# Kernel optimization log

Hardware: AMD Instinct MI355X
Metric: run time of the kernel (lower is better)

## Reference

```python
import jax, jax.numpy as jnp
import numpy as np

B, T, D, H, C = 256, 256, 512, 1024, 128  # batch, steps, input_size, hidden, num_classes


def setup_inputs() -> dict:
    key = jax.random.key(0)
    ks = jax.random.split(key, 8)
    gru_inputs = jax.random.normal(ks[0], (B, T, D), dtype=jnp.float32)
    true_ids = jax.random.randint(ks[1], (B, T), 0, C)
    true_seq = jax.nn.one_hot(true_ids, C, dtype=jnp.float32)
    s = 1.0 / np.sqrt(H).astype(np.float32)
    W_ih = jax.random.uniform(ks[2], (3 * H, D + C), jnp.float32, -s, s)
    b_ih = jax.random.uniform(ks[3], (3 * H,), jnp.float32, -s, s)
    W_hh = jax.random.uniform(ks[4], (3 * H, H), jnp.float32, -s, s)
    b_hh = jax.random.uniform(ks[5], (3 * H,), jnp.float32, -s, s)
    W_out = jax.random.uniform(ks[6], (C, H), jnp.float32, -s, s)
    b_out = jax.random.uniform(ks[7], (C,), jnp.float32, -s, s)
    return {"gru_inputs": gru_inputs, "true_seq": true_seq, "W_ih": W_ih,
            "b_ih": b_ih, "W_hh": W_hh, "b_hh": b_hh, "W_out": W_out, "b_out": b_out}


def reference(gru_inputs, true_seq, W_ih, b_ih, W_hh, b_hh, W_out, b_out):
    # Teacher-forcing (training) branch of TerminalGRU, dropout=0, bos_idx=None.
    Bb, Tt, _ = gru_inputs.shape
    Cc = true_seq.shape[-1]
    Hh = W_hh.shape[1]
    # prev_y[t] = true_seq[t-1], prev_y[0] = zeros (no BOS)
    prev_y = jnp.concatenate(
        [jnp.zeros((Bb, 1, Cc), gru_inputs.dtype), true_seq[:, :-1]], axis=1)
    inp = jnp.concatenate([gru_inputs, prev_y], axis=-1)  # (B,T,D+C)
    # Precompute input-side gate projections as one big GEMM (faithful math).
    gates_x = jnp.einsum('btd,gd->btg', inp, W_ih) + b_ih  # (B,T,3H)
    xr, xz, xn = jnp.split(gates_x, 3, axis=-1)

    def step(h, xs):
        xr_t, xz_t, xn_t = xs  # each (B,H)
        gh = h @ W_hh.T + b_hh  # (B,3H)
        hr, hz, hn = jnp.split(gh, 3, axis=-1)
        r = jax.nn.sigmoid(xr_t + hr)
        z = jax.nn.sigmoid(xz_t + hz)
        n = jnp.tanh(xn_t + r * hn)
        h_new = (1.0 - z) * n + z * h
        return h_new, h_new

    h0 = jnp.zeros((Bb, Hh), gru_inputs.dtype)
    xs = (xr.transpose(1, 0, 2), xz.transpose(1, 0, 2), xn.transpose(1, 0, 2))
    _, hs = jax.lax.scan(step, h0, xs)  # hs: (T,B,H)
    logits = jnp.einsum('tbh,ch->btc', hs, W_out) + b_out  # (B,T,C)
    return logits
```

## Files before the change

kernel.cpp:

```cpp
#include <hip/hip_runtime.h>


#define DEVI __device__ __forceinline__

typedef __bf16 bf16x8 __attribute__((ext_vector_type(8)));
typedef float f32x4 __attribute__((ext_vector_type(4)));
typedef unsigned long long u64;

static constexpr int Bb = 256, Tt = 256, Dd = 512, Hh = 1024, Cc = 128;
static constexpr int G3 = 3072, DC = 640, TC = 32, NC = Tt / TC;
static constexpr int SLOTS = TC + 1;
static constexpr int LDP = 72;

DEVI unsigned short f2b(float f) {
  union { float f; unsigned u; } v; v.f = f;
  unsigned r = v.u + 0x7FFFu + ((v.u >> 16) & 1u);
  return (unsigned short)(r >> 16);
}
DEVI float b2f(unsigned short h) {
  union { unsigned u; float f; } v; v.u = ((unsigned)h) << 16; return v.f;
}


__global__ __launch_bounds__(256) void k_cvt(const float* __restrict__ x,
                                             unsigned short* __restrict__ o, int n) {
  int i = (blockIdx.x * 256 + threadIdx.x) * 8;
  if (i >= n) return;
  float4 a = *(const float4*)(x + i), b = *(const float4*)(x + i + 4);
  uint4 u;
  u.x = (unsigned)f2b(a.x) | ((unsigned)f2b(a.y) << 16);
  u.y = (unsigned)f2b(a.z) | ((unsigned)f2b(a.w) << 16);
  u.z = (unsigned)f2b(b.x) | ((unsigned)f2b(b.y) << 16);
  u.w = (unsigned)f2b(b.z) | ((unsigned)f2b(b.w) << 16);
  *(uint4*)(o + i) = u;
}

__global__ __launch_bounds__(256) void k_cvt_wa(const float* __restrict__ Wih,
                                                unsigned short* __restrict__ Wa) {
  int u = blockIdx.x * 256 + threadIdx.x;
  int g = u >> 6, d = (u & 63) * 8;
  const float* p = Wih + (size_t)g * DC + d;
  float4 a = *(const float4*)p, b = *(const float4*)(p + 4);
  uint4 o;
  o.x = (unsigned)f2b(a.x) | ((unsigned)f2b(a.y) << 16);
  o.y = (unsigned)f2b(a.z) | ((unsigned)f2b(a.w) << 16);
  o.z = (unsigned)f2b(b.x) | ((unsigned)f2b(b.y) << 16);
  o.w = (unsigned)f2b(b.z) | ((unsigned)f2b(b.w) << 16);
  *(uint4*)(Wa + (size_t)g * Dd + d) = o;
}

__global__ __launch_bounds__(256) void k_cvt_wct(const float* __restrict__ Wih,
                                                 unsigned short* __restrict__ WcT) {
  int g = blockIdx.x * 256 + threadIdx.x;
  int c = blockIdx.y;
  WcT[(size_t)c * G3 + g] = f2b(Wih[(size_t)g * DC + Dd + c]);
}

__global__ __launch_bounds__(256) void k_pid(const float* __restrict__ ts,
                                             int* __restrict__ pid) {
  int bt = blockIdx.x * 256 + threadIdx.x;
  int t = bt & (Tt - 1);
  if (t == 0) { pid[bt] = -1; return; }
  const float* p = ts + (size_t)(bt - 1) * Cc;
  int id = 0;
  for (int c = 0; c < Cc; c += 4) {
    float4 v = *(const float4*)(p + c);
    if (v.x > 0.5f) id = c;
    if (v.y > 0.5f) id = c + 1;
    if (v.z > 0.5f) id = c + 2;
    if (v.w > 0.5f) id = c + 3;
  }
  pid[bt] = id;
}

DEVI void gates_tile(int mi, int ni, const unsigned short* __restrict__ Xb,
                     const unsigned short* __restrict__ Wa,
                     const unsigned short* __restrict__ WcT,
                     const float* __restrict__ bih,
                     const int* __restrict__ pid,
                     unsigned short* __restrict__ gx, int t0c,
                     unsigned short* sA, unsigned short* sB) {
  const int m0 = mi * 128, n0 = ni * 128;
  const int tid = threadIdx.x;
  const int l = tid & 63, w = tid >> 6;
  const int wm = w >> 1, wn = w & 1;
  const int r0l = 64 * wm, c0l = 64 * wn;
  const int lr = l & 15, lk = (l >> 4) * 8;

  int srow[4], sq[4];
  size_t gA[4], gB[4];
#pragma unroll
  for (int c = 0; c < 4; ++c) {
    int ch = tid + c * 256;
    srow[c] = ch >> 3; sq[c] = ch & 7;
    int mrow = m0 + srow[c];
    gA[c] = ((size_t)((mrow >> 5) * Tt + t0c + (mrow & 31))) * Dd + sq[c] * 8;
    gB[c] = (size_t)(n0 + srow[c]) * Dd + sq[c] * 8;
  }

  f32x4 acc[4][4] = {};
  for (int ks = 0; ks < 8; ++ks) {
    int k0 = ks * 64;
    __syncthreads();
#pragma unroll
    for (int c = 0; c < 4; ++c) {
      bf16x8 av = *(const bf16x8*)(Xb + gA[c] + k0);
      bf16x8 bv = *(const bf16x8*)(Wa + gB[c] + k0);
      *(bf16x8*)(sA + srow[c] * LDP + sq[c] * 8) = av;
      *(bf16x8*)(sB + srow[c] * LDP + sq[c] * 8) = bv;
    }
    __syncthreads();
#pragma unroll
    for (int kk = 0; kk < 2; ++kk) {
      int kc = kk * 32 + lk;
      bf16x8 a[4], b[4];
#pragma unroll
      for (int mf = 0; mf < 4; ++mf)
        a[mf] = *(const bf16x8*)(sA + (r0l + 16 * mf + lr) * LDP + kc);
#pragma unroll
      for (int nf = 0; nf < 4; ++nf)
        b[nf] = *(const bf16x8*)(sB + (c0l + 16 * nf + lr) * LDP + kc);
#pragma unroll
      for (int mf = 0; mf < 4; ++mf)
#pragma unroll
        for (int nf = 0; nf < 4; ++nf)
          acc[mf][nf] = __builtin_amdgcn_mfma_f32_16x16x32_bf16(a[mf], b[nf], acc[mf][nf], 0, 0, 0);
    }
  }

  const int ri = (l >> 4) * 4;
  const int r0 = m0 + 64 * wm, c0 = n0 + 64 * wn;
  for (int mf = 0; mf < 4; ++mf) {
    int rowb = r0 + 16 * mf + ri;
    int pd[4];
#pragma unroll
    for (int i = 0; i < 4; ++i) {
      int rr = rowb + i;
      pd[i] = pid[(size_t)(rr >> 5) * Tt + t0c + (rr & 31)];
    }
    for (int nf = 0; nf < 4; ++nf) {
      int g = c0 + 16 * nf + lr;
      float bi = bih[g];
#pragma unroll
      for (int i = 0; i < 4; ++i) {
        float v = acc[mf][nf][i] + bi;
        if (pd[i] >= 0) v += b2f(WcT[(size_t)pd[i] * G3 + g]);
        gx[(size_t)(rowb + i) * G3 + g] = f2b(v);
      }
    }
  }
}

__global__ __launch_bounds__(256) void k_gates(const unsigned short* __restrict__ Xb,
                                               const unsigned short* __restrict__ Wa,
                                               const unsigned short* __restrict__ WcT,
                                               const float* __restrict__ bih,
                                               const int* __restrict__ pid,
                                               unsigned short* __restrict__ gx, int t0c) {
  __shared__ unsigned short sA[128 * LDP], sB[128 * LDP];
  gates_tile(blockIdx.x, blockIdx.y, Xb, Wa, WcT, bih, pid, gx, t0c, sA, sB);
}

DEVI void logits_tile(int blk, const unsigned short* __restrict__ hring,
                      const unsigned short* __restrict__ Wo,
                      const float* __restrict__ bout,
                      float* __restrict__ out, int t0) {
  int l = threadIdx.x & 63, w = threadIdx.x >> 6;
  int lr = l & 15, lk = (l >> 4) * 8;
  int r0 = blk * 64 + 16 * w;
  int am = r0 + lr;
  int ab = am >> 5, atl = am & 31;
  const unsigned short* arow =
      hring + (size_t)((t0 + atl + 1) % SLOTS) * (Bb * Hh) + (size_t)ab * Hh;
  f32x4 acc[8] = {};
  for (int kk = 0; kk < 32; ++kk) {
    int k = kk * 32 + lk;
    bf16x8 a = *(const bf16x8*)(arow + k);
#pragma unroll
    for (int nf = 0; nf < 8; ++nf) {
      bf16x8 b = *(const bf16x8*)(Wo + (size_t)(16 * nf + lr) * Hh + k);
      acc[nf] = __builtin_amdgcn_mfma_f32_16x16x32_bf16(a, b, acc[nf], 0, 0, 0);
    }
  }
  int ri = (l >> 4) * 4;
  for (int nf = 0; nf < 8; ++nf) {
    int c = 16 * nf + lr;
    float bo = bout[c];
#pragma unroll
    for (int i = 0; i < 4; ++i) {
      int m = r0 + ri + i;
      int grow = (m >> 5) * Tt + t0 + (m & 31);
      out[(size_t)grow * Cc + c] = acc[nf][i] + bo;
    }
  }
}

__global__ __launch_bounds__(256) void k_combo(
    const unsigned short* __restrict__ Xb, const unsigned short* __restrict__ Wa,
    const unsigned short* __restrict__ WcT, const float* __restrict__ bih,
    const int* __restrict__ pid, unsigned short* __restrict__ gxNext, int doGates,
    const unsigned short* __restrict__ hring, const unsigned short* __restrict__ Wob,
    const float* __restrict__ bou, float* __restrict__ outp, int t0) {
  __shared__ unsigned short sA[128 * LDP], sB[128 * LDP];
  int bid = blockIdx.x;
  if (bid < 1536) {
    if (doGates)
      gates_tile(bid & 63, bid >> 6, Xb, Wa, WcT, bih, pid, gxNext, t0 + TC, sA, sB);
  } else {
    logits_tile(bid - 1536, hring, Wob, bou, outp, t0);
  }
}

__global__ __launch_bounds__(256, 1) void k_scan(const unsigned short* __restrict__ Whh,
                                                 const float* __restrict__ bhh,
                                                 const unsigned short* __restrict__ gx,
                                                 unsigned short* __restrict__ hring,
                                                 unsigned int* __restrict__ notify,
                                                 int t0) {
  __shared__ float red[4 * 32 * 100];
  const int tid = threadIdx.x;
  const int l = tid & 63, w = tid >> 6;
  const int bid = blockIdx.x;
  const int mg = bid & 7, cb = bid >> 3;
  const int lr = l & 15, lk = (l >> 4) * 8;
  const int hcolBase = 32 * cb;
  const int ri = (l >> 4) * 4;

  bf16x8 Breg[6][8];
#pragma unroll
  for (int nf = 0; nf < 6; ++nf) {
    int wrow = (nf >> 1) * Hh + hcolBase + (nf & 1) * 16 + lr;
#pragma unroll
    for (int kk = 0; kk < 8; ++kk) {
      int k = 256 * w + 32 * kk + lk;
      Breg[nf][kk] = *(const bf16x8*)(Whh + (size_t)wrow * Hh + k);
    }
  }

  const int erow = tid >> 3, ej0 = (tid & 7) * 4;
  const int eb = 32 * mg + erow;
  const int ecol = hcolBase + ej0;
  const float4 bhr4 = *(const float4*)(bhh + ecol);
  const float4 bhz4 = *(const float4*)(bhh + Hh + ecol);
  const float4 bhn4 = *(const float4*)(bhh + 2 * Hh + ecol);

  u64 hsave = 0;

  for (int tl = 0; tl < TC; ++tl) {
    const int t = t0 + tl;
    const unsigned short* hcur = hring + (size_t)(t % SLOTS) * (Bb * Hh);
    u64* hnq = (u64*)hring + (size_t)((t + 1) % SLOTS) * (Bb * Hh / 4);

    const size_t gxo = (size_t)(eb * TC + tl) * G3;
    uint2 gr = *(const uint2*)(gx + gxo + ecol);
    uint2 gz = *(const uint2*)(gx + gxo + Hh + ecol);
    uint2 gn = *(const uint2*)(gx + gxo + 2 * Hh + ecol);

    if (t > 0) {
      const unsigned int* np = notify + (mg << 6) + 8 * w + (l & 7);
      for (;;) {
        unsigned int v = __hip_atomic_load(np, __ATOMIC_RELAXED,
                                           __HIP_MEMORY_SCOPE_AGENT);
        if (__all((int)(v >= (unsigned)t))) break;
      }
    }
    asm volatile("" ::: "memory");

    u64 hprev = (tl == 0) ? *(const u64*)(hcur + (size_t)eb * Hh + ecol) : hsave;

    f32x4 acc[2][6] = {};
#pragma unroll
    for (int kk = 0; kk < 8; ++kk) {
      int k = 256 * w + 32 * kk + lk;
      bf16x8 a[2];
#pragma unroll
      for (int mf = 0; mf < 2; ++mf)
        a[mf] = *(const bf16x8*)(hcur + (size_t)(32 * mg + 16 * mf + lr) * Hh + k);
#pragma unroll
      for (int mf = 0; mf < 2; ++mf)
#pragma unroll
        for (int nf = 0; nf < 6; ++nf)
          acc[mf][nf] = __builtin_amdgcn_mfma_f32_16x16x32_bf16(a[mf], Breg[nf][kk], acc[mf][nf], 0, 0, 0);
    }

#pragma unroll
    for (int mf = 0; mf < 2; ++mf)
#pragma unroll
      for (int nf = 0; nf < 6; ++nf)
#pragma unroll
        for (int i = 0; i < 4; ++i)
          red[(w * 32 + 16 * mf + ri + i) * 100 + (nf >> 1) * 32 + (nf & 1) * 16 + lr] = acc[mf][nf][i];
    __syncthreads();

    f32x4 vr = {}, vz = {}, vn = {};
#pragma unroll
    for (int w2 = 0; w2 < 4; ++w2) {
      const float* rp = &red[(w2 * 32 + erow) * 100];
      vr += *(const f32x4*)(rp + ej0);
      vz += *(const f32x4*)(rp + 32 + ej0);
      vn += *(const f32x4*)(rp + 64 + ej0);
    }
    unsigned short grs[4] = {(unsigned short)gr.x, (unsigned short)(gr.x >> 16),
                             (unsigned short)gr.y, (unsigned short)(gr.y >> 16)};
    unsigned short gzs[4] = {(unsigned short)gz.x, (unsigned short)(gz.x >> 16),
                             (unsigned short)gz.y, (unsigned short)(gz.y >> 16)};
    unsigned short gns[4] = {(unsigned short)gn.x, (unsigned short)(gn.x >> 16),
                             (unsigned short)gn.y, (unsigned short)(gn.y >> 16)};
    u64 ho = 0;
#pragma unroll
    for (int i = 0; i < 4; ++i) {
      float hr = vr[i] + (&bhr4.x)[i];
      float hz = vz[i] + (&bhz4.x)[i];
      float hn = vn[i] + (&bhn4.x)[i];
      float xr = b2f(grs[i]), xz = b2f(gzs[i]), xn = b2f(gns[i]);
      float rg = 1.f / (1.f + __expf(-(xr + hr)));
      float zg = 1.f / (1.f + __expf(-(xz + hz)));
      float pre = xn + rg * hn;
      pre = fminf(fmaxf(pre, -15.f), 15.f);
      float e = __expf(-2.f * pre);
      float ng = (1.f - e) / (1.f + e);
      float hp = b2f((unsigned short)(hprev >> (16 * i)));
      float hv = (1.f - zg) * ng + zg * hp;
      ho |= (u64)f2b(hv) << (16 * i);
    }
    __hip_atomic_store(hnq + ((size_t)eb * Hh + ecol) / 4, ho,
                       __ATOMIC_RELAXED, __HIP_MEMORY_SCOPE_AGENT);
    hsave = ho;

    asm volatile("s_waitcnt vmcnt(0)" ::: "memory");
    __syncthreads();
    if (tid == 0)
      __hip_atomic_store(notify + (mg << 6) + cb, (unsigned)(t + 1),
                         __ATOMIC_RELAXED, __HIP_MEMORY_SCOPE_AGENT);
  }
}

extern "C" void kernel_launch(void* const* d_in, const int* in_sizes, int n_in,
                              void* d_out, int out_size, void* d_ws, size_t ws_size,
                              hipStream_t stream) {
  const float* gru = (const float*)d_in[0];
  const float* ts  = (const float*)d_in[1];
  const float* Wih = (const float*)d_in[2];
  const float* bih = (const float*)d_in[3];
  const float* Whh = (const float*)d_in[4];
  const float* bhh = (const float*)d_in[5];
  const float* Wou = (const float*)d_in[6];
  const float* bou = (const float*)d_in[7];
  float* out = (float*)d_out;

  char* ws = (char*)d_ws;
  size_t off = 0;
  auto alloc = [&](size_t bytes) -> void* {
    void* p = ws + off;
    off += (bytes + 255) & ~(size_t)255;
    return p;
  };
  unsigned short* Wa    = (unsigned short*)alloc((size_t)G3 * Dd * 2);
  unsigned short* WcT   = (unsigned short*)alloc((size_t)Cc * G3 * 2);
  unsigned short* Whb   = (unsigned short*)alloc((size_t)G3 * Hh * 2);
  unsigned short* Wob   = (unsigned short*)alloc((size_t)Cc * Hh * 2);
  int*            pid   = (int*)alloc((size_t)Bb * Tt * 4);
  unsigned short* hring = (unsigned short*)alloc((size_t)SLOTS * Bb * Hh * 2);
  unsigned int*   nfy   = (unsigned int*)alloc((size_t)8 * 64 * 4);
  unsigned short* Xb    = (unsigned short*)alloc((size_t)Bb * Tt * Dd * 2);
  unsigned short* gx    = (unsigned short*)alloc((size_t)Bb * TC * G3 * 2);
  if (ws_size < off) return;

  int nX = Bb * Tt * Dd;
  k_cvt<<<nX / 2048, 256, 0, stream>>>(gru, Xb, nX);
  k_cvt<<<(G3 * Hh) / 2048, 256, 0, stream>>>(Whh, Whb, G3 * Hh);
  k_cvt<<<(Cc * Hh) / 2048, 256, 0, stream>>>(Wou, Wob, Cc * Hh);
  k_cvt_wa<<<(G3 * 64) / 256, 256, 0, stream>>>(Wih, Wa);
  k_cvt_wct<<<dim3(G3 / 256, Cc), 256, 0, stream>>>(Wih, WcT);
  k_pid<<<(Bb * Tt) / 256, 256, 0, stream>>>(ts, pid);
  hipMemsetAsync(hring, 0, (size_t)Bb * Hh * 2, stream);
  hipMemsetAsync(nfy, 0, (size_t)8 * 64 * 4, stream);

  k_gates<<<dim3(64, 24), 256, 0, stream>>>(Xb, Wa, WcT, bih, pid, gx, 0);

  for (int c = 0; c < NC; ++c) {
    int t0 = c * TC;
    k_scan<<<dim3(256), dim3(256), 0, stream>>>(Whb, bhh, gx, hring, nfy, t0);
    k_combo<<<dim3(1664), dim3(256), 0, stream>>>(
        Xb, Wa, WcT, bih, pid, gx, (c + 1 < NC) ? 1 : 0,
        hring, Wob, bou, out, t0);
  }
}
```

Before: 2.326 ms.

## Replace notify-counter spin barrier with poisoned hidden-state sentinel polling

Removes the per-block notify counters and the vmcnt wait before the flag store. Each wave instead spins with atomic loads directly on the hidden-state ring, which is pre-filled with an all-ones sentinel, until none of the values it needs are poisoned. It then feeds those loaded values straight into the MFMAs. This folds the flag round-trip into the data load, at the cost of an extra poison kernel per chunk, heavier polling traffic, and reliance on 64-bit stores being seen atomically.

```diff
diff --git a/kernel.cpp b/kernel.cpp
--- a/kernel.cpp
+++ b/kernel.cpp
@@ -11,6 +11,7 @@
 static constexpr int G3 = 3072, DC = 640, TC = 32, NC = Tt / TC;
 static constexpr int SLOTS = TC + 1;
 static constexpr int LDP = 72;
+static constexpr u64 POIS = 0xFFFFFFFFFFFFFFFFull;
 
 DEVI unsigned short f2b(float f) {
   union { float f; unsigned u; } v; v.f = f;
@@ -20,6 +21,8 @@
 DEVI float b2f(unsigned short h) {
   union { unsigned u; float f; } v; v.u = ((unsigned)h) << 16; return v.f;
 }
+
+union HQ { u64 q[2]; bf16x8 v; };
 
 
 __global__ __launch_bounds__(256) void k_cvt(const float* __restrict__ x,
@@ -71,6 +74,15 @@
     if (v.w > 0.5f) id = c + 3;
   }
   pid[bt] = id;
+}
+
+__global__ __launch_bounds__(256) void k_poison(u64* __restrict__ hring, int t0) {
+  int sidx = blockIdx.x >> 6;
+  int slot = (t0 + 1 + sidx) % SLOTS;
+  u64* p = hring + (size_t)slot * (Bb * Hh / 4)
+         + (size_t)(blockIdx.x & 63) * 1024 + (size_t)threadIdx.x * 4;
+  uint4 v; v.x = v.y = v.z = v.w = 0xFFFFFFFFu;
+  *(uint4*)p = v;
 }
 
 DEVI void gates_tile(int mi, int ni, const unsigned short* __restrict__ Xb,
@@ -215,7 +227,6 @@
                                                  const float* __restrict__ bhh,
                                                  const unsigned short* __restrict__ gx,
                                                  unsigned short* __restrict__ hring,
-                                                 unsigned int* __restrict__ notify,
                                                  int t0) {
   __shared__ float red[4 * 32 * 100];
   const int tid = threadIdx.x;
@@ -256,31 +267,44 @@
     uint2 gz = *(const uint2*)(gx + gxo + Hh + ecol);
     uint2 gn = *(const uint2*)(gx + gxo + 2 * Hh + ecol);
 
-    if (t > 0) {
-      const unsigned int* np = notify + (mg << 6) + 8 * w + (l & 7);
-      for (;;) {
-        unsigned int v = __hip_atomic_load(np, __ATOMIC_RELAXED,
-                                           __HIP_MEMORY_SCOPE_AGENT);
-        if (__all((int)(v >= (unsigned)t))) break;
+    u64 hprev = (tl == 0) ? *(const u64*)(hcur + (size_t)eb * Hh + ecol) : hsave;
+
+    f32x4 acc[2][6] = {};
+    const u64* base0 = (const u64*)hcur + ((size_t)(32 * mg + lr) << 8);
+    const u64* base1 = base0 + (16 << 8);
+    const int kq = 64 * w + (lk >> 2);
+#pragma unroll
+    for (int bt = 0; bt < 2; ++bt) {
+      u64 q0[4][2], q1[4][2];
+      int done = 0;
+      for (int it = 0; it < (1 << 18) && !done; ++it) {
+        int ok = 1;
+#pragma unroll
+        for (int j = 0; j < 4; ++j) {
+          int o = kq + 8 * (4 * bt + j);
+          q0[j][0] = __hip_atomic_load(base0 + o,     __ATOMIC_RELAXED, __HIP_MEMORY_SCOPE_AGENT);
+          q0[j][1] = __hip_atomic_load(base0 + o + 1, __ATOMIC_RELAXED, __HIP_MEMORY_SCOPE_AGENT);
+          q1[j][0] = __hip_atomic_load(base1 + o,     __ATOMIC_RELAXED, __HIP_MEMORY_SCOPE_AGENT);
+          q1[j][1] = __hip_atomic_load(base1 + o + 1, __ATOMIC_RELAXED, __HIP_MEMORY_SCOPE_AGENT);
+        }
+#pragma unroll
+        for (int j = 0; j < 4; ++j)
+          ok &= (int)((q0[j][0] != POIS) & (q0[j][1] != POIS) &
+                      (q1[j][0] != POIS) & (q1[j][1] != POIS));
+        done = __all(ok);
       }
-    }
-    asm volatile("" ::: "memory");
-
-    u64 hprev = (tl == 0) ? *(const u64*)(hcur + (size_t)eb * Hh + ecol) : hsave;
-
-    f32x4 acc[2][6] = {};
-#pragma unroll
-    for (int kk = 0; kk < 8; ++kk) {
-      int k = 256 * w + 32 * kk + lk;
-      bf16x8 a[2];
-#pragma unroll
-      for (int mf = 0; mf < 2; ++mf)
-        a[mf] = *(const bf16x8*)(hcur + (size_t)(32 * mg + 16 * mf + lr) * Hh + k);
-#pragma unroll
-      for (int mf = 0; mf < 2; ++mf)
-#pragma unroll
-        for (int nf = 0; nf < 6; ++nf)
-          acc[mf][nf] = __builtin_amdgcn_mfma_f32_16x16x32_bf16(a[mf], Breg[nf][kk], acc[mf][nf], 0, 0, 0);
+#pragma unroll
+      for (int j = 0; j < 4; ++j) {
+        HQ h0, h1;
+        h0.q[0] = q0[j][0]; h0.q[1] = q0[j][1];
+        h1.q[0] = q1[j][0]; h1.q[1] = q1[j][1];
+        int kk = 4 * bt + j;
+#pragma unroll
+        for (int nf = 0; nf < 6; ++nf) {
+          acc[0][nf] = __builtin_amdgcn_mfma_f32_16x16x32_bf16(h0.v, Breg[nf][kk], acc[0][nf], 0, 0, 0);
+          acc[1][nf] = __builtin_amdgcn_mfma_f32_16x16x32_bf16(h1.v, Breg[nf][kk], acc[1][nf], 0, 0, 0);
+        }
+      }
     }
 
 #pragma unroll
@@ -327,11 +351,7 @@
                        __ATOMIC_RELAXED, __HIP_MEMORY_SCOPE_AGENT);
     hsave = ho;
 
-    asm volatile("s_waitcnt vmcnt(0)" ::: "memory");
     __syncthreads();
-    if (tid == 0)
-      __hip_atomic_store(notify + (mg << 6) + cb, (unsigned)(t + 1),
-                         __ATOMIC_RELAXED, __HIP_MEMORY_SCOPE_AGENT);
   }
 }
 
@@ -361,7 +381,6 @@
   unsigned short* Wob   = (unsigned short*)alloc((size_t)Cc * Hh * 2);
   int*            pid   = (int*)alloc((size_t)Bb * Tt * 4);
   unsigned short* hring = (unsigned short*)alloc((size_t)SLOTS * Bb * Hh * 2);
-  unsigned int*   nfy   = (unsigned int*)alloc((size_t)8 * 64 * 4);
   unsigned short* Xb    = (unsigned short*)alloc((size_t)Bb * Tt * Dd * 2);
   unsigned short* gx    = (unsigned short*)alloc((size_t)Bb * TC * G3 * 2);
   if (ws_size < off) return;
@@ -373,14 +392,17 @@
   k_cvt_wa<<<(G3 * 64) / 256, 256, 0, stream>>>(Wih, Wa);
   k_cvt_wct<<<dim3(G3 / 256, Cc), 256, 0, stream>>>(Wih, WcT);
   k_pid<<<(Bb * Tt) / 256, 256, 0, stream>>>(ts, pid);
-  hipMemsetAsync(hring, 0, (size_t)Bb * Hh * 2, stream);
-  hipMemsetAsync(nfy, 0, (size_t)8 * 64 * 4, stream);
+  size_t slotB = (size_t)Bb * Hh * 2;
+  hipMemsetAsync(hring, 0, slotB, stream);
+  hipMemsetAsync((char*)hring + slotB, 0xFF, 32 * slotB, stream);
 
   k_gates<<<dim3(64, 24), 256, 0, stream>>>(Xb, Wa, WcT, bih, pid, gx, 0);
 
   for (int c = 0; c < NC; ++c) {
     int t0 = c * TC;
-    k_scan<<<dim3(256), dim3(256), 0, stream>>>(Whb, bhh, gx, hring, nfy, t0);
+    if (c > 0)
+      k_poison<<<dim3(2048), dim3(256), 0, stream>>>((u64*)hring, t0);
+    k_scan<<<dim3(256), dim3(256), 0, stream>>>(Whb, bhh, gx, hring, t0);
     k_combo<<<dim3(1664), dim3(256), 0, stream>>>(
         Xb, Wa, WcT, bih, pid, gx, (c + 1 < NC) ? 1 : 0,
         hring, Wob, bou, out, t0);
```

Result: slower. 2.736 ms (+17.6%).
